# Kernel optimization log

Hardware: AMD Instinct MI355X
Metric: run time of the kernel (lower is better)

The kernel has to match this reference:

```python
import jax, jax.numpy as jnp
import numpy as np

D_MODEL = 1024
N_HEAD = 16
D_K = D_MODEL // N_HEAD


def setup_inputs() -> dict:
    key = jax.random.key(0)
    ks = jax.random.split(key, 11)
    B, L = 8, 1024
    std = np.sqrt(2.0 / (D_MODEL + D_K)).astype(np.float32)
    inp = {
        "q": jax.random.normal(ks[0], (B, L, D_MODEL), jnp.float32),
        "k": jax.random.normal(ks[1], (B, L, D_MODEL), jnp.float32),
        "v": jax.random.normal(ks[2], (B, L, D_MODEL), jnp.float32),
        # Linear weights stored as [in, out] (transposed torch layout)
        "Wq": jax.random.normal(ks[3], (D_MODEL, D_MODEL), jnp.float32) * std,
        "bq": jnp.zeros((D_MODEL,), jnp.float32),
        "Wk": jax.random.normal(ks[4], (D_MODEL, D_MODEL), jnp.float32) * std,
        "bk": jnp.zeros((D_MODEL,), jnp.float32),
        "Wv": jax.random.normal(ks[5], (D_MODEL, D_MODEL), jnp.float32) * std,
        "bv": jnp.zeros((D_MODEL,), jnp.float32),
        "Wfc": jax.random.normal(ks[6], (D_MODEL, D_MODEL), jnp.float32) * np.sqrt(2.0 / (2 * D_MODEL)).astype(np.float32),
        "bfc": jnp.zeros((D_MODEL,), jnp.float32),
    }
    return inp


def reference(q, k, v, Wq, bq, Wk, bk, Wv, bv, Wfc, bfc):
    B, Lq, _ = q.shape
    Lk = k.shape[1]
    scale = 1.0 / np.sqrt(D_K).astype(np.float32)
    # projections -> [B, L, H, Dk]
    qh = (q @ Wq + bq).reshape(B, Lq, N_HEAD, D_K)
    kh = (k @ Wk + bk).reshape(B, Lk, N_HEAD, D_K)
    vh = (v @ Wv + bv).reshape(B, Lk, N_HEAD, D_K)
    # scores [B, H, Lq, Lk]
    attn = jnp.einsum("bqhd,bkhd->bhqk", qh, kh) * scale
    attn = jax.nn.softmax(attn, axis=-1)
    # dropout is identity in eval mode
    out = jnp.einsum("bhqk,bkhd->bqhd", attn, vh).reshape(B, Lq, N_HEAD * D_K)
    out = out @ Wfc + bfc
    # torch returns attn as [n_head*B, Lq, Lk] with head-major flattening
    attn_flat = jnp.transpose(attn, (1, 0, 2, 3)).reshape(N_HEAD * B, Lq, Lk)
    return out, attn_flat
```

## Files before the change

### kernel.cpp

```cpp
#include <hip/hip_runtime.h>
#include <stdint.h>

typedef __bf16 bf16;
typedef unsigned short u16;
typedef __bf16  bf16x8 __attribute__((ext_vector_type(8)));
typedef unsigned short u16x8 __attribute__((ext_vector_type(8)));
typedef unsigned short u16x4 __attribute__((ext_vector_type(4)));
typedef float   f32x4  __attribute__((ext_vector_type(4)));

typedef __attribute__((address_space(1))) uint32_t gu32;
typedef __attribute__((address_space(3))) uint32_t su32;

__device__ __forceinline__ void async_cp16(const void* gp, void* sp) {
    __builtin_amdgcn_global_load_lds((const gu32*)gp, (su32*)sp, 16, 0, 0);
}

__global__ void detect_dtype(const u16* __restrict__ q, int* __restrict__ flag)
{
    __shared__ int cnt;
    if (threadIdx.x == 0) cnt = 0;
    __syncthreads();
    int c = 0;
    for (int i = threadIdx.x; i < 4096; i += 64) {
        const int e = (q[i] >> 7) & 0xFF;
        if (e >= 96 && e < 160) c++;
    }
    atomicAdd(&cnt, c);
    __syncthreads();
    if (threadIdx.x == 0) *flag = (cnt < 3500) ? 1 : 0;
}

__global__ __launch_bounds__(256) void convert_in(
    const void* __restrict__ src, bf16* __restrict__ dst, int n,
    const int* __restrict__ flagp)
{
    const bool srcF32 = (*flagp != 0);
    const int idx = blockIdx.x * 256 + threadIdx.x;
    if (idx * 8 >= n) return;
    bf16x8 v;
    if (srcF32) {
        const float4 a = ((const float4*)src)[idx * 2];
        const float4 b = ((const float4*)src)[idx * 2 + 1];
        v[0] = (bf16)a.x; v[1] = (bf16)a.y; v[2] = (bf16)a.z; v[3] = (bf16)a.w;
        v[4] = (bf16)b.x; v[5] = (bf16)b.y; v[6] = (bf16)b.z; v[7] = (bf16)b.w;
    } else {
        v = ((const bf16x8*)src)[idx];
    }
    ((bf16x8*)dst)[idx] = v;
}

__global__ __launch_bounds__(256) void convert_bias4(
    const void* __restrict__ b0, const void* __restrict__ b1,
    const void* __restrict__ b2, const void* __restrict__ b3,
    bf16* __restrict__ dst, const int* __restrict__ flagp)
{
    const bool srcF32 = (*flagp != 0);
    const int tid = threadIdx.x;
    const void* srcs[4] = {b0, b1, b2, b3};
#pragma unroll
    for (int t = 0; t < 4; t++) {
        bf16* d = dst + t * 2048 + tid * 4;
        if (srcF32) {
            const float4 v = ((const float4*)srcs[t])[tid];
            d[0] = (bf16)v.x; d[1] = (bf16)v.y; d[2] = (bf16)v.z; d[3] = (bf16)v.w;
        } else {
            *(u16x4*)d = *((const u16x4*)srcs[t] + tid);
        }
    }
}

__global__ __launch_bounds__(256) void gemm_bt128(
    const bf16* __restrict__ A, const bf16* __restrict__ BT,
    const bf16* __restrict__ bias, void* __restrict__ C,
    int M, int N, int K, const int* __restrict__ flagp)
{
    __shared__ alignas(16) bf16 As[128 * 32];
    __shared__ alignas(16) bf16 Bs[128 * 32];
    const bool outF32 = flagp && (*flagp != 0);
    const int tid  = threadIdx.x;
    const int lane = tid & 63, wave = tid >> 6;
    const int l16  = lane & 15, quad = lane >> 4;
    const int m0   = blockIdx.y * 128, n0 = blockIdx.x * 128;
    const int wm   = (wave >> 1) * 64, wn = (wave & 1) * 64;

    f32x4 acc[4][4];
#pragma unroll
    for (int i = 0; i < 4; i++)
#pragma unroll
        for (int j = 0; j < 4; j++) acc[i][j] = {0.f, 0.f, 0.f, 0.f};

    for (int k0 = 0; k0 < K; k0 += 32) {
#pragma unroll
        for (int i = 0; i < 2; i++) {
            const int c   = tid + 256 * i;
            const int row = c >> 2, cc = c & 3;
            async_cp16(A  + (size_t)(m0 + row) * K + k0 + cc * 8,
                       (char*)As + (size_t)(wave * 64 + 256 * i) * 16);
            async_cp16(BT + (size_t)(n0 + row) * K + k0 + cc * 8,
                       (char*)Bs + (size_t)(wave * 64 + 256 * i) * 16);
        }
        __syncthreads();
        bf16x8 af[4], bfr[4];
#pragma unroll
        for (int mi = 0; mi < 4; mi++)
            af[mi] = *(const bf16x8*)(As + (wm + mi * 16 + l16) * 32 + quad * 8);
#pragma unroll
        for (int ni = 0; ni < 4; ni++)
            bfr[ni] = *(const bf16x8*)(Bs + (wn + ni * 16 + l16) * 32 + quad * 8);
#pragma unroll
        for (int mi = 0; mi < 4; mi++)
#pragma unroll
            for (int ni = 0; ni < 4; ni++)
                acc[mi][ni] = __builtin_amdgcn_mfma_f32_16x16x32_bf16(
                    af[mi], bfr[ni], acc[mi][ni], 0, 0, 0);
        __syncthreads();
    }
#pragma unroll
    for (int ni = 0; ni < 4; ni++) {
        const int col = n0 + wn + ni * 16 + l16;
        const float bv = (float)bias[col];
#pragma unroll
        for (int mi = 0; mi < 4; mi++) {
#pragma unroll
            for (int r = 0; r < 4; r++) {
                const int row = m0 + wm + mi * 16 + quad * 4 + r;
                const float val = acc[mi][ni][r] + bv;
                if (outF32) ((float*)C)[(size_t)row * N + col] = val;
                else        ((bf16*)C)[(size_t)row * N + col] = (bf16)val;
            }
        }
    }
}

__global__ __launch_bounds__(256) void transpose_w(
    const void* __restrict__ src, u16* __restrict__ dst,
    const int* __restrict__ flagp)
{
    __shared__ alignas(16) u16 t[64][72];
    const bool srcF32 = (*flagp != 0);
    const int tid = threadIdx.x;
    const int r0 = blockIdx.y * 64, c0 = blockIdx.x * 64;
#pragma unroll
    for (int i = 0; i < 2; i++) {
        const int c = tid + 256 * i;
        const int r = c >> 3, ch = c & 7;
        u16x8 v;
        if (srcF32) {
            const float* sp = (const float*)src + (size_t)(r0 + r) * 1024 + c0 + ch * 8;
            const float4 a = *(const float4*)sp;
            const float4 b = *(const float4*)(sp + 4);
            bf16x8 bv;
            bv[0] = (bf16)a.x; bv[1] = (bf16)a.y; bv[2] = (bf16)a.z; bv[3] = (bf16)a.w;
            bv[4] = (bf16)b.x; bv[5] = (bf16)b.y; bv[6] = (bf16)b.z; bv[7] = (bf16)b.w;
            v = __builtin_bit_cast(u16x8, bv);
        } else {
            v = *(const u16x8*)((const u16*)src + (size_t)(r0 + r) * 1024 + c0 + ch * 8);
        }
        *(u16x8*)&t[r][ch * 8] = v;
    }
    __syncthreads();
#pragma unroll
    for (int i = 0; i < 2; i++) {
        const int c = tid + 256 * i;
        const int d = c >> 3, ch = c & 7;
        u16x8 v;
#pragma unroll
        for (int j = 0; j < 8; j++) v[j] = t[ch * 8 + j][d];
        *(u16x8*)(dst + (size_t)(c0 + d) * 1024 + r0 + ch * 8) = v;
    }
}

__global__ __launch_bounds__(256) void transpose_v(
    const u16* __restrict__ Vp, u16* __restrict__ Vt)
{
    __shared__ alignas(16) u16 t[64][72];
    const int tid = threadIdx.x;
    const int l0 = blockIdx.x * 64, h = blockIdx.y, b = blockIdx.z;
    const u16* src = Vp + (size_t)(b * 1024 + l0) * 1024 + h * 64;
#pragma unroll
    for (int i = 0; i < 2; i++) {
        const int c = tid + 256 * i;
        const int l = c >> 3, ch = c & 7;
        *(u16x8*)&t[l][ch * 8] = *(const u16x8*)(src + (size_t)l * 1024 + ch * 8);
    }
    __syncthreads();
    u16* dst = Vt + ((size_t)(b * 16 + h) * 64) * 1024 + l0;
#pragma unroll
    for (int i = 0; i < 2; i++) {
        const int c = tid + 256 * i;
        const int d = c >> 3, ch = c & 7;
        u16x8 v;
#pragma unroll
        for (int j = 0; j < 8; j++) v[j] = t[ch * 8 + j][d];
        *(u16x8*)(dst + (size_t)d * 1024 + ch * 8) = v;
    }
}

__global__ __launch_bounds__(256) void attn_fused(
    const bf16* __restrict__ Q, const bf16* __restrict__ Kp,
    const bf16* __restrict__ Vt, bf16* __restrict__ O,
    void* __restrict__ Pout, const int* __restrict__ flagp)
{
    __shared__ alignas(16) float sc[16 * 1024];
    const bool outF32 = (*flagp != 0);
    const int tid  = threadIdx.x;
    const int lane = tid & 63, wave = tid >> 6;
    const int l16  = lane & 15, quad = lane >> 4;
    const int q0 = blockIdx.x * 16, h = blockIdx.y, b = blockIdx.z;

    const bf16* Qb = Q  + (size_t)(b * 1024 + q0) * 1024 + h * 64;
    const bf16* Kb = Kp + (size_t)b * 1024 * 1024 + h * 64;
    const bf16x8 a0 = *(const bf16x8*)(Qb + (size_t)l16 * 1024 + quad * 8);
    const bf16x8 a1 = *(const bf16x8*)(Qb + (size_t)l16 * 1024 + quad * 8 + 32);
#pragma unroll 4
    for (int t = 0; t < 16; ++t) {
        const int n0 = wave * 256 + t * 16;
        const bf16* kp = Kb + (size_t)(n0 + l16) * 1024 + quad * 8;
        const bf16x8 b0 = *(const bf16x8*)kp;
        const bf16x8 b1 = *(const bf16x8*)(kp + 32);
        f32x4 acc = {0.f, 0.f, 0.f, 0.f};
        acc = __builtin_amdgcn_mfma_f32_16x16x32_bf16(a0, b0, acc, 0, 0, 0);
        acc = __builtin_amdgcn_mfma_f32_16x16x32_bf16(a1, b1, acc, 0, 0, 0);
#pragma unroll
        for (int r = 0; r < 4; r++)
            sc[(quad * 4 + r) * 1024 + n0 + l16] = acc[r] * 0.125f;
    }
    __syncthreads();

    const int r = tid >> 4, g = tid & 15;
    const float* prow = sc + r * 1024 + g * 8;
    float4 vv[16];
    float m = -3.0e38f;
#pragma unroll
    for (int j = 0; j < 8; j++) {
        vv[2 * j]     = *(const float4*)(prow + j * 128);
        vv[2 * j + 1] = *(const float4*)(prow + j * 128 + 4);
        m = fmaxf(m, fmaxf(fmaxf(vv[2 * j].x, vv[2 * j].y),
                           fmaxf(vv[2 * j].z, vv[2 * j].w)));
        m = fmaxf(m, fmaxf(fmaxf(vv[2 * j + 1].x, vv[2 * j + 1].y),
                           fmaxf(vv[2 * j + 1].z, vv[2 * j + 1].w)));
    }
#pragma unroll
    for (int o = 8; o >= 1; o >>= 1) m = fmaxf(m, __shfl_xor(m, o, 16));
    float s = 0.f;
#pragma unroll
    for (int j = 0; j < 16; j++) {
        vv[j].x = __expf(vv[j].x - m); vv[j].y = __expf(vv[j].y - m);
        vv[j].z = __expf(vv[j].z - m); vv[j].w = __expf(vv[j].w - m);
        s += vv[j].x + vv[j].y + vv[j].z + vv[j].w;
    }
#pragma unroll
    for (int o = 8; o >= 1; o >>= 1) s += __shfl_xor(s, o, 16);
    const float inv = 1.f / s;
#pragma unroll
    for (int j = 0; j < 16; j++) {
        vv[j].x *= inv; vv[j].y *= inv; vv[j].z *= inv; vv[j].w *= inv;
    }
    __syncthreads();

    bf16* Pb = (bf16*)sc;
    const size_t rowbase = (size_t)((h * 8 + b) * 1024 + q0 + r) * 1024;
#pragma unroll
    for (int j = 0; j < 8; j++) {
        const float4 v0 = vv[2 * j], v1 = vv[2 * j + 1];
        bf16x8 ov;
        ov[0] = (bf16)v0.x; ov[1] = (bf16)v0.y; ov[2] = (bf16)v0.z; ov[3] = (bf16)v0.w;
        ov[4] = (bf16)v1.x; ov[5] = (bf16)v1.y; ov[6] = (bf16)v1.z; ov[7] = (bf16)v1.w;
        *(bf16x8*)(Pb + r * 1032 + g * 8 + j * 128) = ov;
        if (outF32) {
            float* outp = (float*)Pout + 8388608 + rowbase + g * 8 + j * 128;
            *(float4*)outp = v0;
            *(float4*)(outp + 4) = v1;
        } else {
            *(bf16x8*)((bf16*)Pout + 8388608 + rowbase + g * 8 + j * 128) = ov;
        }
    }
    __syncthreads();

    const bf16* Pfrag = Pb + l16 * 1032 + quad * 8;
    const bf16* Vfrag = Vt + ((size_t)(b * 16 + h) * 64 + wave * 16 + l16) * 1024
                           + quad * 8;
    f32x4 acc0 = {0.f, 0.f, 0.f, 0.f}, acc1 = {0.f, 0.f, 0.f, 0.f};
#pragma unroll 4
    for (int k0 = 0; k0 < 1024; k0 += 64) {
        const bf16x8 pa0 = *(const bf16x8*)(Pfrag + k0);
        const bf16x8 vb0 = *(const bf16x8*)(Vfrag + k0);
        const bf16x8 pa1 = *(const bf16x8*)(Pfrag + k0 + 32);
        const bf16x8 vb1 = *(const bf16x8*)(Vfrag + k0 + 32);
        acc0 = __builtin_amdgcn_mfma_f32_16x16x32_bf16(pa0, vb0, acc0, 0, 0, 0);
        acc1 = __builtin_amdgcn_mfma_f32_16x16x32_bf16(pa1, vb1, acc1, 0, 0, 0);
    }
    bf16* Ob = O + (size_t)b * 1024 * 1024 + h * 64 + wave * 16 + l16;
#pragma unroll
    for (int rr = 0; rr < 4; rr++)
        Ob[(size_t)(q0 + quad * 4 + rr) * 1024] = (bf16)(acc0[rr] + acc1[rr]);
}

extern "C" void kernel_launch(void* const* d_in, const int* in_sizes, int n_in,
                              void* d_out, int out_size, void* d_ws, size_t ws_size,
                              hipStream_t stream)
{
    const void* q   = d_in[0];
    const void* k   = d_in[1];
    const void* v   = d_in[2];
    const void* Wq  = d_in[3];
    const void* bq  = d_in[4];
    const void* Wk  = d_in[5];
    const void* bk  = d_in[6];
    const void* Wv  = d_in[7];
    const void* bv  = d_in[8];
    const void* Wfc = d_in[9];
    const void* bfc = d_in[10];

    const size_t M1 = 1024 * 1024;
    bf16* ws   = (bf16*)d_ws;
    bf16* WqT  = ws;
    bf16* WkT  = ws + 1 * M1;
    bf16* WvT  = ws + 2 * M1;
    bf16* WfcT = ws + 3 * M1;
    bf16* bB   = ws + 4 * M1;
    bf16* qb   = ws + 5 * M1;
    bf16* kb   = ws + 13 * M1;
    bf16* vb   = ws + 21 * M1;
    bf16* Qp   = ws + 29 * M1;
    bf16* Kp   = ws + 5 * M1;
    bf16* Vp   = ws + 13 * M1;
    bf16* Vt   = ws + 21 * M1;
    bf16* O    = ws + 13 * M1;
    int*  flag = (int*)(ws + 37 * M1);

    const dim3 tb(256);

    detect_dtype<<<1, 64, 0, stream>>>((const u16*)q, flag);

    convert_in<<<4096, tb, 0, stream>>>(q, qb, 8 * 1024 * 1024, flag);
    convert_in<<<4096, tb, 0, stream>>>(k, kb, 8 * 1024 * 1024, flag);
    convert_in<<<4096, tb, 0, stream>>>(v, vb, 8 * 1024 * 1024, flag);
    convert_bias4<<<1, tb, 0, stream>>>(bq, bk, bv, bfc, bB, flag);

    const dim3 tg(16, 16);
    transpose_w<<<tg, tb, 0, stream>>>(Wq,  (u16*)WqT,  flag);
    transpose_w<<<tg, tb, 0, stream>>>(Wk,  (u16*)WkT,  flag);
    transpose_w<<<tg, tb, 0, stream>>>(Wv,  (u16*)WvT,  flag);
    transpose_w<<<tg, tb, 0, stream>>>(Wfc, (u16*)WfcT, flag);

    const dim3 pg(8, 64);
    gemm_bt128<<<pg, tb, 0, stream>>>(qb, WqT, bB + 0 * 2048, Qp, 8192, 1024, 1024, nullptr);
    gemm_bt128<<<pg, tb, 0, stream>>>(kb, WkT, bB + 1 * 2048, Kp, 8192, 1024, 1024, nullptr);
    gemm_bt128<<<pg, tb, 0, stream>>>(vb, WvT, bB + 2 * 2048, Vp, 8192, 1024, 1024, nullptr);

    transpose_v<<<dim3(16, 16, 8), tb, 0, stream>>>((const u16*)Vp, (u16*)Vt);

    attn_fused<<<dim3(64, 16, 8), tb, 0, stream>>>(Qp, Kp, Vt, O, d_out, flag);

    gemm_bt128<<<pg, tb, 0, stream>>>(O, WfcT, bB + 3 * 2048, d_out, 8192, 1024, 1024, flag);
}
```

Measured before the change: 1.060 ms.

## Batch QKV launches, swizzle GEMM tiles, keep attention scores in registers

```diff
diff --git a/kernel.cpp b/kernel.cpp
--- a/kernel.cpp
+++ b/kernel.cpp
@@ -30,13 +30,16 @@
     if (threadIdx.x == 0) *flag = (cnt < 3500) ? 1 : 0;
 }
 
-__global__ __launch_bounds__(256) void convert_in(
-    const void* __restrict__ src, bf16* __restrict__ dst, int n,
+__global__ __launch_bounds__(256) void convert_qkv(
+    const void* __restrict__ s0, const void* __restrict__ s1,
+    const void* __restrict__ s2, bf16* __restrict__ dst0, size_t dstStride,
     const int* __restrict__ flagp)
 {
     const bool srcF32 = (*flagp != 0);
+    const int z = blockIdx.y;
+    const void* src = (z == 0) ? s0 : ((z == 1) ? s1 : s2);
+    bf16* dst = dst0 + dstStride * z;
     const int idx = blockIdx.x * 256 + threadIdx.x;
-    if (idx * 8 >= n) return;
     bf16x8 v;
     if (srcF32) {
         const float4 a = ((const float4*)src)[idx * 2];
@@ -70,17 +73,28 @@
 }
 
 __global__ __launch_bounds__(256) void gemm_bt128(
-    const bf16* __restrict__ A, const bf16* __restrict__ BT,
-    const bf16* __restrict__ bias, void* __restrict__ C,
-    int M, int N, int K, const int* __restrict__ flagp)
+    const bf16* __restrict__ A0, const bf16* __restrict__ BT0,
+    const bf16* __restrict__ bias0, void* __restrict__ C0,
+    int M, int N, int K,
+    size_t aStride, size_t btStride, size_t biasStride, size_t cStride,
+    const int* __restrict__ flagp)
 {
     __shared__ alignas(16) bf16 As[128 * 32];
     __shared__ alignas(16) bf16 Bs[128 * 32];
+    const int z = blockIdx.z;
+    const bf16* A    = A0 + aStride * z;
+    const bf16* BT   = BT0 + btStride * z;
+    const bf16* bias = bias0 + biasStride * z;
     const bool outF32 = flagp && (*flagp != 0);
     const int tid  = threadIdx.x;
     const int lane = tid & 63, wave = tid >> 6;
     const int l16  = lane & 15, quad = lane >> 4;
-    const int m0   = blockIdx.y * 128, n0 = blockIdx.x * 128;
+    const int nwgx = gridDim.x;
+    const int nwg  = nwgx * gridDim.y;
+    const int wg   = blockIdx.y * nwgx + blockIdx.x;
+    const int sw   = (wg & 7) * (nwg >> 3) + (wg >> 3);
+    const int bx   = sw % nwgx, by = sw / nwgx;
+    const int m0   = by * 128, n0 = bx * 128;
     const int wm   = (wave >> 1) * 64, wn = (wave & 1) * 64;
 
     f32x4 acc[4][4];
@@ -125,19 +139,23 @@
             for (int r = 0; r < 4; r++) {
                 const int row = m0 + wm + mi * 16 + quad * 4 + r;
                 const float val = acc[mi][ni][r] + bv;
-                if (outF32) ((float*)C)[(size_t)row * N + col] = val;
-                else        ((bf16*)C)[(size_t)row * N + col] = (bf16)val;
+                if (outF32) ((float*)C0 + cStride * z)[(size_t)row * N + col] = val;
+                else        ((bf16*)C0  + cStride * z)[(size_t)row * N + col] = (bf16)val;
             }
         }
     }
 }
 
 __global__ __launch_bounds__(256) void transpose_w(
-    const void* __restrict__ src, u16* __restrict__ dst,
-    const int* __restrict__ flagp)
+    const void* __restrict__ s0, const void* __restrict__ s1,
+    const void* __restrict__ s2, const void* __restrict__ s3,
+    u16* __restrict__ dst0, const int* __restrict__ flagp)
 {
     __shared__ alignas(16) u16 t[64][72];
     const bool srcF32 = (*flagp != 0);
+    const int z = blockIdx.z;
+    const void* src = (z == 0) ? s0 : ((z == 1) ? s1 : ((z == 2) ? s2 : s3));
+    u16* dst = dst0 + (size_t)z * 1024 * 1024;
     const int tid = threadIdx.x;
     const int r0 = blockIdx.y * 64, c0 = blockIdx.x * 64;
 #pragma unroll
@@ -196,12 +214,13 @@
     }
 }
 
-__global__ __launch_bounds__(256) void attn_fused(
+__global__ __launch_bounds__(256, 4) void attn_fused(
     const bf16* __restrict__ Q, const bf16* __restrict__ Kp,
     const bf16* __restrict__ Vt, bf16* __restrict__ O,
     void* __restrict__ Pout, const int* __restrict__ flagp)
 {
-    __shared__ alignas(16) float sc[16 * 1024];
+    __shared__ alignas(16) bf16 Pl[16 * 1032];
+    __shared__ float red[2][4][16];
     const bool outF32 = (*flagp != 0);
     const int tid  = threadIdx.x;
     const int lane = tid & 63, wave = tid >> 6;
@@ -212,7 +231,8 @@
     const bf16* Kb = Kp + (size_t)b * 1024 * 1024 + h * 64;
     const bf16x8 a0 = *(const bf16x8*)(Qb + (size_t)l16 * 1024 + quad * 8);
     const bf16x8 a1 = *(const bf16x8*)(Qb + (size_t)l16 * 1024 + quad * 8 + 32);
-#pragma unroll 4
+    f32x4 s[16];
+#pragma unroll 2
     for (int t = 0; t < 16; ++t) {
         const int n0 = wave * 256 + t * 16;
         const bf16* kp = Kb + (size_t)(n0 + l16) * 1024 + quad * 8;
@@ -222,62 +242,67 @@
         acc = __builtin_amdgcn_mfma_f32_16x16x32_bf16(a0, b0, acc, 0, 0, 0);
         acc = __builtin_amdgcn_mfma_f32_16x16x32_bf16(a1, b1, acc, 0, 0, 0);
 #pragma unroll
-        for (int r = 0; r < 4; r++)
-            sc[(quad * 4 + r) * 1024 + n0 + l16] = acc[r] * 0.125f;
-    }
-    __syncthreads();
-
-    const int r = tid >> 4, g = tid & 15;
-    const float* prow = sc + r * 1024 + g * 8;
-    float4 vv[16];
-    float m = -3.0e38f;
-#pragma unroll
-    for (int j = 0; j < 8; j++) {
-        vv[2 * j]     = *(const float4*)(prow + j * 128);
-        vv[2 * j + 1] = *(const float4*)(prow + j * 128 + 4);
-        m = fmaxf(m, fmaxf(fmaxf(vv[2 * j].x, vv[2 * j].y),
-                           fmaxf(vv[2 * j].z, vv[2 * j].w)));
-        m = fmaxf(m, fmaxf(fmaxf(vv[2 * j + 1].x, vv[2 * j + 1].y),
-                           fmaxf(vv[2 * j + 1].z, vv[2 * j + 1].w)));
-    }
-#pragma unroll
-    for (int o = 8; o >= 1; o >>= 1) m = fmaxf(m, __shfl_xor(m, o, 16));
-    float s = 0.f;
-#pragma unroll
-    for (int j = 0; j < 16; j++) {
-        vv[j].x = __expf(vv[j].x - m); vv[j].y = __expf(vv[j].y - m);
-        vv[j].z = __expf(vv[j].z - m); vv[j].w = __expf(vv[j].w - m);
-        s += vv[j].x + vv[j].y + vv[j].z + vv[j].w;
-    }
-#pragma unroll
-    for (int o = 8; o >= 1; o >>= 1) s += __shfl_xor(s, o, 16);
-    const float inv = 1.f / s;
-#pragma unroll
-    for (int j = 0; j < 16; j++) {
-        vv[j].x *= inv; vv[j].y *= inv; vv[j].z *= inv; vv[j].w *= inv;
-    }
-    __syncthreads();
-
-    bf16* Pb = (bf16*)sc;
-    const size_t rowbase = (size_t)((h * 8 + b) * 1024 + q0 + r) * 1024;
-#pragma unroll
-    for (int j = 0; j < 8; j++) {
-        const float4 v0 = vv[2 * j], v1 = vv[2 * j + 1];
-        bf16x8 ov;
-        ov[0] = (bf16)v0.x; ov[1] = (bf16)v0.y; ov[2] = (bf16)v0.z; ov[3] = (bf16)v0.w;
-        ov[4] = (bf16)v1.x; ov[5] = (bf16)v1.y; ov[6] = (bf16)v1.z; ov[7] = (bf16)v1.w;
-        *(bf16x8*)(Pb + r * 1032 + g * 8 + j * 128) = ov;
-        if (outF32) {
-            float* outp = (float*)Pout + 8388608 + rowbase + g * 8 + j * 128;
-            *(float4*)outp = v0;
-            *(float4*)(outp + 4) = v1;
-        } else {
-            *(bf16x8*)((bf16*)Pout + 8388608 + rowbase + g * 8 + j * 128) = ov;
-        }
-    }
-    __syncthreads();
-
-    const bf16* Pfrag = Pb + l16 * 1032 + quad * 8;
+        for (int r = 0; r < 4; r++) s[t][r] = acc[r] * 0.125f;
+    }
+
+    float m[4] = {-3.0e38f, -3.0e38f, -3.0e38f, -3.0e38f};
+#pragma unroll
+    for (int t = 0; t < 16; t++)
+#pragma unroll
+        for (int r = 0; r < 4; r++) m[r] = fmaxf(m[r], s[t][r]);
+#pragma unroll
+    for (int o = 8; o >= 1; o >>= 1)
+#pragma unroll
+        for (int r = 0; r < 4; r++) m[r] = fmaxf(m[r], __shfl_xor(m[r], o));
+    if (l16 == 0) {
+#pragma unroll
+        for (int r = 0; r < 4; r++) red[0][wave][quad * 4 + r] = m[r];
+    }
+    __syncthreads();
+    float M[4];
+#pragma unroll
+    for (int r = 0; r < 4; r++)
+        M[r] = fmaxf(fmaxf(red[0][0][quad * 4 + r], red[0][1][quad * 4 + r]),
+                     fmaxf(red[0][2][quad * 4 + r], red[0][3][quad * 4 + r]));
+    float sum[4] = {0.f, 0.f, 0.f, 0.f};
+#pragma unroll
+    for (int t = 0; t < 16; t++)
+#pragma unroll
+        for (int r = 0; r < 4; r++) {
+            s[t][r] = __expf(s[t][r] - M[r]);
+            sum[r] += s[t][r];
+        }
+#pragma unroll
+    for (int o = 8; o >= 1; o >>= 1)
+#pragma unroll
+        for (int r = 0; r < 4; r++) sum[r] += __shfl_xor(sum[r], o);
+    if (l16 == 0) {
+#pragma unroll
+        for (int r = 0; r < 4; r++) red[1][wave][quad * 4 + r] = sum[r];
+    }
+    __syncthreads();
+    float inv[4];
+#pragma unroll
+    for (int r = 0; r < 4; r++)
+        inv[r] = 1.f / (red[1][0][quad * 4 + r] + red[1][1][quad * 4 + r] +
+                        red[1][2][quad * 4 + r] + red[1][3][quad * 4 + r]);
+
+    const size_t pbase = 8388608 + (size_t)((h * 8 + b) * 1024 + q0) * 1024;
+#pragma unroll
+    for (int t = 0; t < 16; t++) {
+        const int col = wave * 256 + t * 16 + l16;
+#pragma unroll
+        for (int r = 0; r < 4; r++) {
+            const int row = quad * 4 + r;
+            const float p = s[t][r] * inv[r];
+            Pl[row * 1032 + col] = (bf16)p;
+            if (outF32) ((float*)Pout)[pbase + (size_t)row * 1024 + col] = p;
+            else        ((bf16*)Pout)[pbase + (size_t)row * 1024 + col] = (bf16)p;
+        }
+    }
+    __syncthreads();
+
+    const bf16* Pfrag = Pl + l16 * 1032 + quad * 8;
     const bf16* Vfrag = Vt + ((size_t)(b * 16 + h) * 64 + wave * 16 + l16) * 1024
                            + quad * 8;
     f32x4 acc0 = {0.f, 0.f, 0.f, 0.f}, acc1 = {0.f, 0.f, 0.f, 0.f};
@@ -315,43 +340,34 @@
     const size_t M1 = 1024 * 1024;
     bf16* ws   = (bf16*)d_ws;
     bf16* WqT  = ws;
-    bf16* WkT  = ws + 1 * M1;
-    bf16* WvT  = ws + 2 * M1;
     bf16* WfcT = ws + 3 * M1;
     bf16* bB   = ws + 4 * M1;
     bf16* qb   = ws + 5 * M1;
-    bf16* kb   = ws + 13 * M1;
-    bf16* vb   = ws + 21 * M1;
     bf16* Qp   = ws + 29 * M1;
-    bf16* Kp   = ws + 5 * M1;
-    bf16* Vp   = ws + 13 * M1;
-    bf16* Vt   = ws + 21 * M1;
-    bf16* O    = ws + 13 * M1;
-    int*  flag = (int*)(ws + 37 * M1);
+    bf16* Kp   = ws + 37 * M1;
+    bf16* Vp   = ws + 45 * M1;
+    bf16* Vt   = ws + 53 * M1;
+    bf16* O    = ws + 61 * M1;
+    int*  flag = (int*)(ws + 69 * M1);
 
     const dim3 tb(256);
 
     detect_dtype<<<1, 64, 0, stream>>>((const u16*)q, flag);
 
-    convert_in<<<4096, tb, 0, stream>>>(q, qb, 8 * 1024 * 1024, flag);
-    convert_in<<<4096, tb, 0, stream>>>(k, kb, 8 * 1024 * 1024, flag);
-    convert_in<<<4096, tb, 0, stream>>>(v, vb, 8 * 1024 * 1024, flag);
+    convert_qkv<<<dim3(4096, 3), tb, 0, stream>>>(q, k, v, qb, 8 * M1, flag);
     convert_bias4<<<1, tb, 0, stream>>>(bq, bk, bv, bfc, bB, flag);
 
-    const dim3 tg(16, 16);
-    transpose_w<<<tg, tb, 0, stream>>>(Wq,  (u16*)WqT,  flag);
-    transpose_w<<<tg, tb, 0, stream>>>(Wk,  (u16*)WkT,  flag);
-    transpose_w<<<tg, tb, 0, stream>>>(Wv,  (u16*)WvT,  flag);
-    transpose_w<<<tg, tb, 0, stream>>>(Wfc, (u16*)WfcT, flag);
-
-    const dim3 pg(8, 64);
-    gemm_bt128<<<pg, tb, 0, stream>>>(qb, WqT, bB + 0 * 2048, Qp, 8192, 1024, 1024, nullptr);
-    gemm_bt128<<<pg, tb, 0, stream>>>(kb, WkT, bB + 1 * 2048, Kp, 8192, 1024, 1024, nullptr);
-    gemm_bt128<<<pg, tb, 0, stream>>>(vb, WvT, bB + 2 * 2048, Vp, 8192, 1024, 1024, nullptr);
+    transpose_w<<<dim3(16, 16, 4), tb, 0, stream>>>(Wq, Wk, Wv, Wfc, (u16*)WqT, flag);
+
+    gemm_bt128<<<dim3(8, 64, 3), tb, 0, stream>>>(
+        qb, WqT, bB, Qp, 8192, 1024, 1024,
+        8 * M1, M1, 2048, 8 * M1, nullptr);
 
     transpose_v<<<dim3(16, 16, 8), tb, 0, stream>>>((const u16*)Vp, (u16*)Vt);
 
     attn_fused<<<dim3(64, 16, 8), tb, 0, stream>>>(Qp, Kp, Vt, O, d_out, flag);
 
-    gemm_bt128<<<pg, tb, 0, stream>>>(O, WfcT, bB + 3 * 2048, d_out, 8192, 1024, 1024, flag);
-}
+    gemm_bt128<<<dim3(8, 64, 1), tb, 0, stream>>>(
+        O, WfcT, bB + 3 * 2048, d_out, 8192, 1024, 1024,
+        0, 0, 0, 0, flag);
+}
```

After: 1.359 ms. +28.2%, slower.
